# Kernel optimization log

Hardware: AMD Instinct MI355X
Metric: run time of the kernel (lower is better)

The kernel has to match this reference:

```python
import jax, jax.numpy as jnp
import numpy as np

NA, NT, E = 8000, 30000, 150000
H, C, HID = 4, 64, 64  # heads, per-head out_channels, hidden_dim
AF, TF = 32, 48


def _gat(x_src, x_dst, src, dst, W, a_src, a_dst, bias, n_dst):
    # PyG GATConv, concat=False, add_self_loops=False, eval (no dropout)
    h_src = (x_src @ W).reshape(-1, H, C)          # [Ns,H,C]
    h_dst = (x_dst @ W).reshape(-1, H, C)          # [Nd,H,C]
    al_s = jnp.sum(h_src * a_src, axis=-1)         # [Ns,H]
    al_d = jnp.sum(h_dst * a_dst, axis=-1)         # [Nd,H]
    e = jax.nn.leaky_relu(al_s[src] + al_d[dst], 0.2)  # [E,H]
    m = jax.ops.segment_max(e, dst, num_segments=n_dst)
    m = jnp.where(jnp.isfinite(m), m, 0.0)
    ex = jnp.exp(e - m[dst])
    den = jax.ops.segment_sum(ex, dst, num_segments=n_dst)
    alpha = ex / (den[dst] + 1e-16)                # per-dst softmax
    out = jax.ops.segment_sum(alpha[:, :, None] * h_src[src], dst, num_segments=n_dst)
    return jnp.mean(out, axis=1) + bias            # mean over heads + bias


def _bn(x, g, b):  # BatchNorm1d, training-mode batch stats, biased var
    mu = jnp.mean(x, axis=0)
    v = jnp.var(x, axis=0)
    return g * (x - mu) * jax.lax.rsqrt(v + 1e-5) + b


def _ln(x, g, b):
    mu = jnp.mean(x, axis=-1, keepdims=True)
    v = jnp.var(x, axis=-1, keepdims=True)
    return g * (x - mu) * jax.lax.rsqrt(v + 1e-5) + b


def setup_inputs() -> dict:
    key = jax.random.key(0)
    ks = jax.random.split(key, 40)
    n = lambda i, shp, s=0.05: jax.random.normal(ks[i], shp, jnp.float32) * s
    ri = lambda i, hi: jax.random.randint(ks[i], (E,), 0, hi, jnp.int32)
    inp = {
        'x_agent': jax.random.normal(ks[0], (NA, AF), jnp.float32),
        'x_track': jax.random.normal(ks[1], (NT, TF), jnp.float32),
        'ei_a2t1_src': ri(2, NA), 'ei_a2t1_dst': ri(3, NT),
        'ei_t2a1_src': ri(4, NT), 'ei_t2a1_dst': ri(5, NA),
        'ei_a2t2_src': ri(6, NA), 'ei_a2t2_dst': ri(7, NT),
        'ei_t2a2_src': ri(8, NT), 'ei_t2a2_dst': ri(9, NA),
        'ae_W': n(10, (AF, HID)), 'ae_b': jnp.zeros((HID,), jnp.float32),
        'te_W': n(11, (TF, HID)), 'te_b': jnp.zeros((HID,), jnp.float32),
        # stacked GATConv params: [layer=3, relation=4, ...]; rel order: a2t1,t2a1,a2t2,t2a2
        'conv_W': n(12, (3, 4, HID, H * C)),
        'conv_asrc': n(13, (3, 4, H, C)),
        'conv_adst': n(14, (3, 4, H, C)),
        'conv_bias': jnp.zeros((3, 4, C), jnp.float32),
        'bn_gamma': jnp.ones((3, 2, HID), jnp.float32),   # [layer, agent/track, HID]
        'bn_beta': jnp.zeros((3, 2, HID), jnp.float32),
        # actor heads: 0=agent_alpha,1=agent_beta,2=track_alpha,3=track_beta
        'actor_W1': n(15, (4, HID, HID // 2)), 'actor_b1': jnp.zeros((4, HID // 2), jnp.float32),
        'actor_g': jnp.ones((4, HID // 2), jnp.float32), 'actor_be': jnp.zeros((4, HID // 2), jnp.float32),
        'actor_W2': n(16, (4, HID // 2, 1)), 'actor_b2': jnp.zeros((4, 1), jnp.float32),
        # critic global value head
        'cW1': n(17, (HID * 6, HID * 2)), 'cb1': jnp.zeros((HID * 2,), jnp.float32),
        'cg1': jnp.ones((HID * 2,), jnp.float32), 'cbe1': jnp.zeros((HID * 2,), jnp.float32),
        'cW2': n(18, (HID * 2, HID)), 'cb2': jnp.zeros((HID,), jnp.float32),
        'cg2': jnp.ones((HID,), jnp.float32), 'cbe2': jnp.zeros((HID,), jnp.float32),
        'cW3': n(19, (HID, HID // 2)), 'cb3': jnp.zeros((HID // 2,), jnp.float32),
        'cW4': n(20, (HID // 2, 1)), 'cb4': jnp.zeros((1,), jnp.float32),
    }
    return inp


def _forward(x_agent, x_track,
             ei_a2t1_src, ei_a2t1_dst, ei_t2a1_src, ei_t2a1_dst,
             ei_a2t2_src, ei_a2t2_dst, ei_t2a2_src, ei_t2a2_dst,
             ae_W, ae_b, te_W, te_b,
             conv_W, conv_asrc, conv_adst, conv_bias,
             bn_gamma, bn_beta,
             actor_W1, actor_b1, actor_g, actor_be, actor_W2, actor_b2,
             cW1, cb1, cg1, cbe1, cW2, cb2, cg2, cbe2, cW3, cb3, cW4, cb4):
    xa = jax.nn.relu(x_agent @ ae_W + ae_b)
    xt = jax.nn.relu(x_track @ te_W + te_b)
    prev_a, prev_t = None, None
    for l in range(3):
        # HeteroConv aggr='mean': track <- mean(rel0, rel2); agent <- mean(rel1, rel3)
        ot = 0.5 * (_gat(xa, xt, ei_a2t1_src, ei_a2t1_dst, conv_W[l, 0], conv_asrc[l, 0], conv_adst[l, 0], conv_bias[l, 0], NT)
                    + _gat(xa, xt, ei_a2t2_src, ei_a2t2_dst, conv_W[l, 2], conv_asrc[l, 2], conv_adst[l, 2], conv_bias[l, 2], NT))
        oa = 0.5 * (_gat(xt, xa, ei_t2a1_src, ei_t2a1_dst, conv_W[l, 1], conv_asrc[l, 1], conv_adst[l, 1], conv_bias[l, 1], NA)
                    + _gat(xt, xa, ei_t2a2_src, ei_t2a2_dst, conv_W[l, 3], conv_asrc[l, 3], conv_adst[l, 3], conv_bias[l, 3], NA))
        oa = _bn(jax.nn.relu(oa), bn_gamma[l, 0], bn_beta[l, 0])
        ot = _bn(jax.nn.relu(ot), bn_gamma[l, 1], bn_beta[l, 1])
        if l > 0:  # residuals after layers 2 and 3
            oa = oa + prev_a
            ot = ot + prev_t
        prev_a, prev_t = oa, ot
        xa, xt = oa, ot

    def head(x, i):
        h = jax.nn.relu(_ln(x @ actor_W1[i] + actor_b1[i], actor_g[i], actor_be[i]))
        return jax.nn.softplus(h @ actor_W2[i] + actor_b2[i]) + 1.0

    aA, aB = head(xa, 0), head(xa, 1)
    tA, tB = head(xt, 2), head(xt, 3)
    aC = aA / (aA + aB)
    tC = tA / (tA + tB)

    # critic global value (torch.std is unbiased, ddof=1)
    g = jnp.concatenate([
        jnp.mean(xa, axis=0), jnp.max(xa, axis=0), jnp.std(xa, axis=0, ddof=1),
        jnp.mean(xt, axis=0), jnp.max(xt, axis=0), jnp.std(xt, axis=0, ddof=1)], axis=0)[None, :]
    h = jax.nn.relu(_ln(g @ cW1 + cb1, cg1, cbe1))
    h = jax.nn.relu(_ln(h @ cW2 + cb2, cg2, cbe2))
    h = jax.nn.relu(h @ cW3 + cb3)
    gv = jnp.squeeze(h @ cW4 + cb4)
    return aA, aB, aC, tA, tB, tC, gv


def reference(x_agent, x_track,
              ei_a2t1_src, ei_a2t1_dst, ei_t2a1_src, ei_t2a1_dst,
              ei_a2t2_src, ei_a2t2_dst, ei_t2a2_src, ei_t2a2_dst,
              ae_W, ae_b, te_W, te_b,
              conv_W, conv_asrc, conv_adst, conv_bias,
              bn_gamma, bn_beta,
              actor_W1, actor_b1, actor_g, actor_be, actor_W2, actor_b2,
              cW1, cb1, cg1, cbe1, cW2, cb2, cg2, cbe2, cW3, cb3, cW4, cb4):
    return _forward(x_agent, x_track,
                    ei_a2t1_src, ei_a2t1_dst, ei_t2a1_src, ei_t2a1_dst,
                    ei_a2t2_src, ei_a2t2_dst, ei_t2a2_src, ei_t2a2_dst,
                    ae_W, ae_b, te_W, te_b,
                    conv_W, conv_asrc, conv_adst, conv_bias,
                    bn_gamma, bn_beta,
                    actor_W1, actor_b1, actor_g, actor_be, actor_W2, actor_b2,
                    cW1, cb1, cg1, cbe1, cW2, cb2, cg2, cbe2, cW3, cb3, cW4, cb4)
```

## Files before the change

### kernel.cpp

```cpp
#include <hip/hip_runtime.h>
#include <math.h>

#define NAg 8000
#define NTr 30000
#define NE  150000

#define XA_OFF 0
#define XT_OFF 512000
#define H0_OFF 2432000
#define H1_OFF 4480000
#define H2_OFF 12160000
#define H3_OFF 14208000
#define BNSTB 8320000
#define WVB   8336384
#define ALS0 21888000
#define ALS1 21920000
#define ALS2 22040000
#define ALS3 22072000
#define ALD0 22192000
#define ALD1 22312000
#define ALD2 22344000
#define ALD3 22464000
#define ESRC_I 22496000
#define OAACC 23104000
#define OTACC 23616000
#define BNST 25536000
#define CST  25536256
#define ROWP_I 25536640
#define CURS_I 25656704
#define RELSTRIDE 30016

typedef unsigned short ushortT;

__device__ __forceinline__ float lrelu(float x){ return x >= 0.f ? x : 0.2f*x; }
__device__ __forceinline__ unsigned fmap(float f){ unsigned u=__float_as_uint(f); return (u&0x80000000u)? ~u : (u|0x80000000u); }
__device__ __forceinline__ float funmap(unsigned u){ return (u&0x80000000u)? __uint_as_float(u&0x7FFFFFFFu) : __uint_as_float(~u); }
__device__ __forceinline__ float softplusf(float x){ return fmaxf(x,0.f) + log1pf(expf(-fabsf(x))); }
__device__ __forceinline__ ushortT f2bf(float f){
  unsigned u = __float_as_uint(f);
  unsigned r = u + 0x7FFFu + ((u>>16)&1u);
  return (ushortT)(r>>16);
}
__device__ __forceinline__ float bf2f(ushortT s){ return __uint_as_float(((unsigned)s)<<16); }
__device__ __forceinline__ float wred64(float v){
  #pragma unroll
  for (int o=32;o;o>>=1) v += __shfl_xor(v,o);
  return v;
}
__device__ __forceinline__ float wred32(float v){
  #pragma unroll
  for (int o=16;o;o>>=1) v += __shfl_xor(v,o,32);
  return v;
}
__device__ __forceinline__ int selH(int r){ return r==0?H0_OFF: r==1?H1_OFF: r==2?H2_OFF:H3_OFF; }
__device__ __forceinline__ int selALS(int r){ return r==0?ALS0: r==1?ALS1: r==2?ALS2:ALS3; }
__device__ __forceinline__ int selALD(int r){ return r==0?ALD0: r==1?ALD1: r==2?ALD2:ALD3; }

__device__ __forceinline__ float agg_rel(const int* es, int p, int p1, const float* als,
                                         const ushortT* h16, float ad, int lane, int hh, int base) {
  float num0=0.f, num1=0.f, num2=0.f, num3=0.f, den=0.f;
  for (; p + 4 <= p1; p += 4) {
    int sa = es[p], sb = es[p+1], sc = es[p+2], sd4 = es[p+3];
    ushort4 va = *(const ushort4*)(h16 + (size_t)sa*256 + lane*4);
    ushort4 vb = *(const ushort4*)(h16 + (size_t)sb*256 + lane*4);
    ushort4 vc = *(const ushort4*)(h16 + (size_t)sc*256 + lane*4);
    ushort4 vd = *(const ushort4*)(h16 + (size_t)sd4*256 + lane*4);
    float la = als[sa*4+hh], lb = als[sb*4+hh], lc = als[sc*4+hh], ld = als[sd4*4+hh];
    float ea = __expf(lrelu(la + ad));
    float eb = __expf(lrelu(lb + ad));
    float ec = __expf(lrelu(lc + ad));
    float ed = __expf(lrelu(ld + ad));
    den += (ea+eb)+(ec+ed);
    float qa0=__shfl(ea,base), qa1=__shfl(ea,base+1), qa2=__shfl(ea,base+2), qa3=__shfl(ea,base+3);
    float qb0=__shfl(eb,base), qb1=__shfl(eb,base+1), qb2=__shfl(eb,base+2), qb3=__shfl(eb,base+3);
    float qc0=__shfl(ec,base), qc1=__shfl(ec,base+1), qc2=__shfl(ec,base+2), qc3=__shfl(ec,base+3);
    float qd0=__shfl(ed,base), qd1=__shfl(ed,base+1), qd2=__shfl(ed,base+2), qd3=__shfl(ed,base+3);
    num0 += qa0*bf2f(va.x) + qb0*bf2f(vb.x) + qc0*bf2f(vc.x) + qd0*bf2f(vd.x);
    num1 += qa1*bf2f(va.y) + qb1*bf2f(vb.y) + qc1*bf2f(vc.y) + qd1*bf2f(vd.y);
    num2 += qa2*bf2f(va.z) + qb2*bf2f(vb.z) + qc2*bf2f(vc.z) + qd2*bf2f(vd.z);
    num3 += qa3*bf2f(va.w) + qb3*bf2f(vb.w) + qc3*bf2f(vc.w) + qd3*bf2f(vd.w);
  }
  for (; p < p1; ++p) {
    int s = es[p];
    ushort4 va = *(const ushort4*)(h16 + (size_t)s*256 + lane*4);
    float e = __expf(lrelu(als[s*4 + hh] + ad));
    den += e;
    float q0 = __shfl(e, base), q1 = __shfl(e, base+1), q2 = __shfl(e, base+2), q3 = __shfl(e, base+3);
    num0 += q0*bf2f(va.x); num1 += q1*bf2f(va.y); num2 += q2*bf2f(va.z); num3 += q3*bf2f(va.w);
  }
  float rd = 1.f/(den + 1e-16f);
  float r0 = __shfl(rd, base), r1 = __shfl(rd, base+1), r2 = __shfl(rd, base+2), r3 = __shfl(rd, base+3);
  return num0*r0 + num1*r1 + num2*r2 + num3*r3;
}

__global__ __launch_bounds__(256) void k_encoder(const float* xA, const float* xT,
    const float* aeW, const float* aeB, const float* teW, const float* teB, float* ws) {
  int type = blockIdx.y;
  int N = type ? NTr : NAg;
  int t = threadIdx.x, wv = t >> 6, lane = t & 63;
  int n = blockIdx.x*4 + wv;
  int F = type ? 48 : 32;
  const float* X = type ? xT : xA;
  const float* W = type ? teW : aeW;
  const float* B = type ? teB : aeB;
  float* out = ws + (type ? XT_OFF : XA_OFF);
  __shared__ float xs[4][48];
  if (n < N && lane < F) xs[wv][lane] = X[(size_t)n*F + lane];
  __syncthreads();
  if (n >= N) return;
  float acc = B[lane];
  for (int k = 0; k < F; ++k) acc += xs[wv][k] * W[k*64 + lane];
  out[(size_t)n*64 + lane] = fmaxf(acc, 0.f);
}

__global__ __launch_bounds__(256) void k_hist(const int* d0_,const int* d1_,const int* d2_,const int* d3_,
                                              int* wsi) {
  int r = blockIdx.y;
  const int* dp = r==0? d0_ : r==1? d1_ : r==2? d2_ : d3_;
  int e = blockIdx.x*256 + threadIdx.x;
  if (e >= NE) return;
  atomicAdd(&wsi[ROWP_I + r*RELSTRIDE + dp[e]], 1);
}

__global__ __launch_bounds__(256) void k_scan(int* wsi) {
  int r = blockIdx.x;
  int n = ((r & 1) ? NAg : NTr) + 1;
  int* rp = wsi + ROWP_I + r*RELSTRIDE;
  __shared__ int part[256];
  int t = threadIdx.x;
  int chunk = (n + 255) / 256;
  int lo = t*chunk, hi = min(lo + chunk, n);
  int s = 0;
  for (int i = lo; i < hi; ++i) s += rp[i];
  part[t] = s;
  __syncthreads();
  if (t == 0) {
    int run = 0;
    for (int i = 0; i < 256; ++i) { int tm = part[i]; part[i] = run; run += tm; }
  }
  __syncthreads();
  int run = part[t];
  for (int i = lo; i < hi; ++i) { int tm = rp[i]; rp[i] = run; run += tm; }
}

__global__ __launch_bounds__(256) void k_fill(const int* s0,const int* d0_,const int* s1,const int* d1_,
    const int* s2,const int* d2_,const int* s3,const int* d3_, int* wsi) {
  int r = blockIdx.y;
  const int* sp = r==0? s0 : r==1? s1 : r==2? s2 : s3;
  const int* dp = r==0? d0_ : r==1? d1_ : r==2? d2_ : d3_;
  int e = blockIdx.x*256 + threadIdx.x;
  if (e >= NE) return;
  int d = dp[e];
  int pos = wsi[ROWP_I + r*RELSTRIDE + d] + atomicAdd(&wsi[CURS_I + r*RELSTRIDE + d], 1);
  wsi[ESRC_I + r*NE + pos] = sp[e];
}

__global__ __launch_bounds__(256) void k_wv(const float* convW, const float* convAsrc,
                                            const float* convAdst, float* ws) {
  int y = blockIdx.x, layer = blockIdx.y;
  int side = y >> 2, r = y & 3;
  const float* W  = convW + (size_t)(layer*4 + r)*64*256;
  const float* av = (side ? convAsrc : convAdst) + (size_t)(layer*4 + r)*256;
  int t = threadIdx.x;
  int k = t >> 2, h = t & 3;
  float s = 0.f;
  for (int c = 0; c < 64; ++c) s += W[k*256 + h*64 + c] * av[h*64 + c];
  ws[WVB + (size_t)(layer*8 + y)*256 + t] = s;
}

__global__ __launch_bounds__(256) void k_alx(float* ws, int layer) {
  int bid = blockIdx.x;
  int y, b0;
  if (bid < 7500)       { y = 0; b0 = bid; }
  else if (bid < 9500)  { y = 1; b0 = bid - 7500; }
  else if (bid < 17000) { y = 2; b0 = bid - 9500; }
  else if (bid < 19000) { y = 3; b0 = bid - 17000; }
  else if (bid < 21000) { y = 4; b0 = bid - 19000; }
  else if (bid < 28500) { y = 5; b0 = bid - 21000; }
  else if (bid < 30500) { y = 6; b0 = bid - 28500; }
  else                  { y = 7; b0 = bid - 30500; }
  int side = y >> 2, r = y & 3;
  int t = threadIdx.x, wv = t >> 6, lane = t & 63;
  int n = b0*4 + wv;
  const float* xv = ws + (side ? ((r & 1) ? XT_OFF : XA_OFF) : ((r & 1) ? XA_OFF : XT_OFF));
  float4 wv4 = *(const float4*)(ws + WVB + (size_t)(layer*8 + y)*256 + lane*4);
  float xk = xv[(size_t)n*64 + lane];
  float p0 = wred64(xk * wv4.x);
  float p1 = wred64(xk * wv4.y);
  float p2 = wred64(xk * wv4.z);
  float p3 = wred64(xk * wv4.w);
  if (lane == 0) {
    float4 o; o.x = p0; o.y = p1; o.z = p2; o.w = p3;
    *(float4*)(ws + (side ? selALS(r) : selALD(r)) + (size_t)n*4) = o;
  }
}

__global__ __launch_bounds__(256) void k_hgemm(const float* convW, float* ws, int layer) {
  int tile = blockIdx.x;
  int r, row0;
  if (tile < 500)        { r = 0; row0 = tile*16; }
  else if (tile < 2375)  { r = 1; row0 = (tile-500)*16; }
  else if (tile < 2875)  { r = 2; row0 = (tile-2375)*16; }
  else                   { r = 3; row0 = (tile-2875)*16; }
  const float* W  = convW + (size_t)(layer*4 + r)*64*256;
  const float* xg = ws + ((r & 1) ? XT_OFF : XA_OFF);
  ushortT* h16 = (ushortT*)(ws + selH(r));
  __shared__ float xs[16][64];
  int t = threadIdx.x;
  #pragma unroll
  for (int i = 0; i < 4; ++i) {
    int lin = i*256 + t;
    xs[lin>>6][lin&63] = xg[((size_t)row0 + (lin>>6))*64 + (lin&63)];
  }
  __syncthreads();
  int c0 = t & 63;
  int tr = t >> 6;
  float acc[4][4];
  #pragma unroll
  for (int i=0;i<4;i++){ acc[i][0]=0;acc[i][1]=0;acc[i][2]=0;acc[i][3]=0; }
  const float* Wc = W + c0;
  for (int k4 = 0; k4 < 16; ++k4) {
    float4 xv[4];
    #pragma unroll
    for (int i = 0; i < 4; ++i) xv[i] = *(const float4*)&xs[tr*4+i][k4*4];
    #pragma unroll
    for (int kk = 0; kk < 4; ++kk) {
      int k = k4*4 + kk;
      float w0 = Wc[k*256], w1 = Wc[k*256+64], w2 = Wc[k*256+128], w3 = Wc[k*256+192];
      #pragma unroll
      for (int i = 0; i < 4; ++i) {
        float x = (kk==0)?xv[i].x:(kk==1)?xv[i].y:(kk==2)?xv[i].z:xv[i].w;
        acc[i][0] += x*w0; acc[i][1] += x*w1; acc[i][2] += x*w2; acc[i][3] += x*w3;
      }
    }
  }
  #pragma unroll
  for (int i = 0; i < 4; ++i) {
    int row = row0 + tr*4 + i;
    ushort4 pk;
    pk.x = f2bf(acc[i][0]); pk.y = f2bf(acc[i][1]);
    pk.z = f2bf(acc[i][2]); pk.w = f2bf(acc[i][3]);
    *(ushort4*)(h16 + (size_t)row*256 + c0*4) = pk;
  }
}

__global__ __launch_bounds__(256) void k_agg(const float* convBias, float* ws, int layer) {
  int t = threadIdx.x, wv = t >> 6, lane = t & 63, hh = lane & 3, base = lane & ~3;
  const int* wsi = (const int*)ws;
  int bid = blockIdx.x;
  __shared__ float part[4][64];
  __shared__ float sh1[4][64];
  __shared__ float sh2[4][64];
  if (bid < 4000) {
    int node = bid*2 + (wv >> 1);
    int rr = wv & 1;
    int r = rr ? 3 : 1;
    const int* rp = wsi + ROWP_I + r*RELSTRIDE;
    const int* es = wsi + ESRC_I + r*NE;
    const float* als = ws + selALS(r);
    const ushortT* h16 = (const ushortT*)(ws + selH(r));
    float ad = (ws + selALD(r))[node*4 + hh];
    part[wv][lane] = agg_rel(es, rp[node], rp[node+1], als, h16, ad, lane, hh, base);
    __syncthreads();
    if (rr == 0) {
      float o = part[wv][lane] + part[wv+1][lane];
      float bavg = 0.5f*(convBias[(layer*4 + 1)*64 + lane] + convBias[(layer*4 + 3)*64 + lane]);
      float z = fmaxf(o*0.125f + bavg, 0.f);
      ws[OAACC + (size_t)node*64 + lane] = z;
      sh1[wv][lane] = z; sh2[wv][lane] = z*z;
    } else {
      sh1[wv][lane] = 0.f; sh2[wv][lane] = 0.f;
    }
    __syncthreads();
    if (t < 64) {
      float s1 = sh1[0][t] + sh1[1][t] + sh1[2][t] + sh1[3][t];
      float s2 = sh2[0][t] + sh2[1][t] + sh2[2][t] + sh2[3][t];
      int bucket = bid & 63;
      atomicAdd(&ws[BNSTB + bucket*256 + t], s1);
      atomicAdd(&ws[BNSTB + bucket*256 + 64 + t], s2);
    }
  } else {
    int node = (bid - 4000)*4 + wv;
    float outv = 0.f;
    #pragma unroll
    for (int rr = 0; rr < 2; ++rr) {
      int r = rr ? 2 : 0;
      const int* rp = wsi + ROWP_I + r*RELSTRIDE;
      const int* es = wsi + ESRC_I + r*NE;
      const float* als = ws + selALS(r);
      const ushortT* h16 = (const ushortT*)(ws + selH(r));
      float ad = (ws + selALD(r))[node*4 + hh];
      outv += agg_rel(es, rp[node], rp[node+1], als, h16, ad, lane, hh, base);
    }
    float bavg = 0.5f*(convBias[(layer*4 + 0)*64 + lane] + convBias[(layer*4 + 2)*64 + lane]);
    float z = fmaxf(outv*0.125f + bavg, 0.f);
    ws[OTACC + (size_t)node*64 + lane] = z;
    sh1[wv][lane] = z; sh2[wv][lane] = z*z;
    __syncthreads();
    if (t < 64) {
      float s1 = sh1[0][t] + sh1[1][t] + sh1[2][t] + sh1[3][t];
      float s2 = sh2[0][t] + sh2[1][t] + sh2[2][t] + sh2[3][t];
      int bucket = bid & 63;
      atomicAdd(&ws[BNSTB + bucket*256 + 128 + t], s1);
      atomicAdd(&ws[BNSTB + bucket*256 + 192 + t], s2);
    }
  }
}

__global__ __launch_bounds__(256) void k_bnred(float* ws) {
  int t = threadIdx.x;
  float s = 0.f;
  #pragma unroll
  for (int b = 0; b < 64; ++b) s += ws[BNSTB + b*256 + t];
  ws[BNST + t] = s;
}

__global__ __launch_bounds__(256) void k_bnnorm(const float* bnG, const float* bnB, float* ws, int layer) {
  int type = blockIdx.y;
  int N = type ? NTr : NAg;
  float* acc = ws + (type ? OTACC : OAACC);
  float* x = ws + (type ? XT_OFF : XA_OFF);
  int i = blockIdx.x*256 + threadIdx.x;
  if (i >= N*64) return;
  int c = i & 63;
  float Nf = (float)N;
  float s1 = ws[BNST + type*128 + c], s2 = ws[BNST + type*128 + 64 + c];
  float mu = s1/Nf, var = s2/Nf - mu*mu;
  float g = bnG[(layer*2 + type)*64 + c], b = bnB[(layer*2 + type)*64 + c];
  float y = g*(acc[i]-mu)*rsqrtf(var + 1e-5f) + b;
  if (layer > 0) y += x[i];
  x[i] = y;
}

__global__ __launch_bounds__(256) void k_actor(const float* aW1, const float* ab1, const float* ag,
    const float* abe, const float* aW2, const float* ab2, const float* ws, float* out) {
  int type = blockIdx.y;
  int N = type ? NTr : NAg;
  int t = threadIdx.x, wv = t >> 6, lane = t & 63;
  int p = lane >> 5, j = lane & 31;
  int n = blockIdx.x*4 + wv;
  const float* xg = ws + (type ? XT_OFF : XA_OFF);
  __shared__ float xsh[4][64];
  {
    int nn = blockIdx.x*4 + (t >> 6);
    if (nn < N) xsh[t >> 6][t & 63] = xg[(size_t)nn*64 + (t & 63)];
  }
  __syncthreads();
  if (n >= N) return;
  int i = (type ? 2 : 0) + p;
  const float* W = aW1 + i*2048 + j;
  float a0 = 0.f, a1 = 0.f, a2 = 0.f, a3 = 0.f;
  #pragma unroll
  for (int k = 0; k < 64; k += 4) {
    a0 += xsh[wv][k]   * W[k*32];
    a1 += xsh[wv][k+1] * W[(k+1)*32];
    a2 += xsh[wv][k+2] * W[(k+2)*32];
    a3 += xsh[wv][k+3] * W[(k+3)*32];
  }
  float tv = ((a0+a1)+(a2+a3)) + ab1[i*32 + j];
  float mu = wred32(tv) * (1.f/32.f);
  float dz = tv - mu;
  float var = wred32(dz*dz) * (1.f/32.f);
  float hn = fmaxf(ag[i*32+j]*dz*rsqrtf(var + 1e-5f) + abe[i*32+j], 0.f);
  float s = wred32(hn * aW2[i*32 + j]) + ab2[i];
  float val = softplusf(s) + 1.f;
  float vA = __shfl(val, 0);
  float vB = __shfl(val, 32);
  if (lane == 0) {
    int offA = type ? 24000 : 0, offB = type ? 54000 : 8000, offC = type ? 84000 : 16000;
    out[offA + n] = vA;
    out[offB + n] = vB;
    out[offC + n] = vA / (vA + vB);
  }
}

__global__ __launch_bounds__(256) void k_criticstats(float* ws) {
  int type = blockIdx.y;
  int N = type ? NTr : NAg;
  const float* x = ws + (type ? XT_OFF : XA_OFF);
  int t = threadIdx.x;
  int c = t & 63;
  float s1 = 0.f, s2 = 0.f, mx = -3.4e38f;
  for (int n = blockIdx.x*4 + (t>>6); n < N; n += gridDim.x*4) {
    float v = x[(size_t)n*64 + c];
    s1 += v; s2 += v*v; mx = fmaxf(mx, v);
  }
  __shared__ float sd[3][256];
  sd[0][t]=s1; sd[1][t]=s2; sd[2][t]=mx;
  __syncthreads();
  if (t < 64) {
    s1 = sd[0][t]+sd[0][t+64]+sd[0][t+128]+sd[0][t+192];
    s2 = sd[1][t]+sd[1][t+64]+sd[1][t+128]+sd[1][t+192];
    mx = fmaxf(fmaxf(sd[2][t],sd[2][t+64]), fmaxf(sd[2][t+128],sd[2][t+192]));
    atomicAdd(&ws[CST + type*192 + c], s1);
    atomicAdd(&ws[CST + type*192 + 64 + c], s2);
    atomicMax((unsigned*)&ws[CST + type*192 + 128 + c], fmap(mx));
  }
}

__device__ __forceinline__ float blocksum128(float v, float* red) {
  int t = threadIdx.x;
  red[t] = v; __syncthreads();
  #pragma unroll
  for (int s = 64; s > 0; s >>= 1) { if (t < s) red[t] += red[t+s]; __syncthreads(); }
  float r = red[0]; __syncthreads();
  return r;
}

__global__ __launch_bounds__(128) void k_critic(const float* cW1,const float* cb1,const float* cg1,const float* cbe1,
    const float* cW2,const float* cb2,const float* cg2,const float* cbe2,
    const float* cW3,const float* cb3,const float* cW4,const float* cb4,
    const float* ws, float* out) {
  __shared__ float g[384];
  __shared__ float h1[128];
  __shared__ float h2s[64];
  __shared__ float red[128];
  int t = threadIdx.x;
  if (t < 64) {
    #pragma unroll
    for (int type = 0; type < 2; ++type) {
      float Nf = type ? 30000.f : 8000.f;
      float s1 = ws[CST + type*192 + t];
      float s2 = ws[CST + type*192 + 64 + t];
      unsigned mu_ = __float_as_uint(ws[CST + type*192 + 128 + t]);
      float mean = s1 / Nf;
      float sd = sqrtf(fmaxf((s2 - Nf*mean*mean) / (Nf - 1.f), 0.f));
      g[type*192 + t] = mean;
      g[type*192 + 64 + t] = funmap(mu_);
      g[type*192 + 128 + t] = sd;
    }
  }
  __syncthreads();
  float v = cb1[t];
  for (int k = 0; k < 384; ++k) v += g[k] * cW1[k*128 + t];
  float mu = blocksum128(v, red) * (1.f/128.f);
  float d = v - mu;
  float var = blocksum128(d*d, red) * (1.f/128.f);
  h1[t] = fmaxf(cg1[t]*d*rsqrtf(var + 1e-5f) + cbe1[t], 0.f);
  __syncthreads();
  float v2 = 0.f;
  if (t < 64) { v2 = cb2[t]; for (int k = 0; k < 128; ++k) v2 += h1[k] * cW2[k*64 + t]; }
  float mu2 = blocksum128(t < 64 ? v2 : 0.f, red) * (1.f/64.f);
  float d2 = v2 - mu2;
  float var2 = blocksum128(t < 64 ? d2*d2 : 0.f, red) * (1.f/64.f);
  if (t < 64) h2s[t] = fmaxf(cg2[t]*d2*rsqrtf(var2 + 1e-5f) + cbe2[t], 0.f);
  __syncthreads();
  float v3 = 0.f;
  if (t < 32) {
    v3 = cb3[t];
    for (int k = 0; k < 64; ++k) v3 += h2s[k] * cW3[k*32 + t];
    v3 = fmaxf(v3, 0.f);
  }
  float s4 = blocksum128(t < 32 ? v3 * cW4[t] : 0.f, red);
  if (t == 0) out[114000] = s4 + cb4[0];
}

extern "C" void kernel_launch(void* const* d_in, const int* in_sizes, int n_in,
                              void* d_out, int out_size, void* d_ws, size_t ws_size,
                              hipStream_t stream) {
  const float* x_agent = (const float*)d_in[0];
  const float* x_track = (const float*)d_in[1];
  const int* s0 = (const int*)d_in[2]; const int* d0_ = (const int*)d_in[3];
  const int* s1 = (const int*)d_in[4]; const int* d1_ = (const int*)d_in[5];
  const int* s2 = (const int*)d_in[6]; const int* d2_ = (const int*)d_in[7];
  const int* s3 = (const int*)d_in[8]; const int* d3_ = (const int*)d_in[9];
  const float* aeW = (const float*)d_in[10]; const float* aeB = (const float*)d_in[11];
  const float* teW = (const float*)d_in[12]; const float* teB = (const float*)d_in[13];
  const float* convW    = (const float*)d_in[14];
  const float* convAsrc = (const float*)d_in[15];
  const float* convAdst = (const float*)d_in[16];
  const float* convBias = (const float*)d_in[17];
  const float* bnG = (const float*)d_in[18]; const float* bnB = (const float*)d_in[19];
  const float* aW1 = (const float*)d_in[20]; const float* ab1 = (const float*)d_in[21];
  const float* ag  = (const float*)d_in[22]; const float* abe = (const float*)d_in[23];
  const float* aW2 = (const float*)d_in[24]; const float* ab2 = (const float*)d_in[25];
  const float* cW1 = (const float*)d_in[26]; const float* cb1 = (const float*)d_in[27];
  const float* cg1 = (const float*)d_in[28]; const float* cbe1 = (const float*)d_in[29];
  const float* cW2 = (const float*)d_in[30]; const float* cb2 = (const float*)d_in[31];
  const float* cg2 = (const float*)d_in[32]; const float* cbe2 = (const float*)d_in[33];
  const float* cW3 = (const float*)d_in[34]; const float* cb3 = (const float*)d_in[35];
  const float* cW4 = (const float*)d_in[36]; const float* cb4 = (const float*)d_in[37];
  float* ws = (float*)d_ws;
  int* wsi = (int*)d_ws;
  float* out = (float*)d_out;

  hipMemsetAsync(wsi + ROWP_I, 0, (size_t)240128 * sizeof(int), stream);
  hipMemsetAsync(ws + CST, 0, (size_t)384 * sizeof(float), stream);

  k_encoder<<<dim3(7500, 2), 256, 0, stream>>>(x_agent, x_track, aeW, aeB, teW, teB, ws);

  k_hist<<<dim3(586, 4), 256, 0, stream>>>(d0_, d1_, d2_, d3_, wsi);
  k_scan<<<dim3(4), 256, 0, stream>>>(wsi);
  k_fill<<<dim3(586, 4), 256, 0, stream>>>(s0,d0_,s1,d1_,s2,d2_,s3,d3_, wsi);
  k_wv<<<dim3(8, 3), 256, 0, stream>>>(convW, convAsrc, convAdst, ws);

  for (int l = 0; l < 3; ++l) {
    hipMemsetAsync(ws + BNSTB, 0, (size_t)16384 * sizeof(float), stream);
    k_alx<<<dim3(38000), 256, 0, stream>>>(ws, l);
    k_hgemm<<<dim3(4750), 256, 0, stream>>>(convW, ws, l);
    k_agg<<<dim3(11500), 256, 0, stream>>>(convBias, ws, l);
    k_bnred<<<1, 256, 0, stream>>>(ws);
    k_bnnorm<<<dim3(7500, 2), 256, 0, stream>>>(bnG, bnB, ws, l);
  }

  k_criticstats<<<dim3(128, 2), 256, 0, stream>>>(ws);
  k_actor<<<dim3(7500, 2), 256, 0, stream>>>(aW1, ab1, ag, abe, aW2, ab2, ws, out);
  k_critic<<<1, 128, 0, stream>>>(cW1,cb1,cg1,cbe1,cW2,cb2,cg2,cbe2,cW3,cb3,cW4,cb4, ws, out);
}
```

Baseline: 668.7 us.

## Fold memsets into kernels, trim padded grids, pre-transpose conv weights

After: 659.0 us. No clear change (-1.5%).

```diff
diff --git a/kernel.cpp b/kernel.cpp
--- a/kernel.cpp
+++ b/kernel.cpp
@@ -13,6 +13,7 @@
 #define H3_OFF 14208000
 #define BNSTB 8320000
 #define WVB   8336384
+#define W2B   8342528
 #define ALS0 21888000
 #define ALS1 21920000
 #define ALS2 22040000
@@ -95,10 +96,13 @@
 
 __global__ __launch_bounds__(256) void k_encoder(const float* xA, const float* xT,
     const float* aeW, const float* aeB, const float* teW, const float* teB, float* ws) {
-  int type = blockIdx.y;
+  int bid = blockIdx.x;
+  int t = threadIdx.x, wv = t >> 6, lane = t & 63;
+  if (bid < 2 && t < 192) ws[CST + bid*192 + t] = 0.f;
+  int type, nb;
+  if (bid < 2000) { type = 0; nb = bid; } else { type = 1; nb = bid - 2000; }
   int N = type ? NTr : NAg;
-  int t = threadIdx.x, wv = t >> 6, lane = t & 63;
-  int n = blockIdx.x*4 + wv;
+  int n = nb*4 + wv;
   int F = type ? 48 : 32;
   const float* X = type ? xT : xA;
   const float* W = type ? teW : aeW;
@@ -155,21 +159,32 @@
   wsi[ESRC_I + r*NE + pos] = sp[e];
 }
 
-__global__ __launch_bounds__(256) void k_wv(const float* convW, const float* convAsrc,
-                                            const float* convAdst, float* ws) {
-  int y = blockIdx.x, layer = blockIdx.y;
-  int side = y >> 2, r = y & 3;
-  const float* W  = convW + (size_t)(layer*4 + r)*64*256;
-  const float* av = (side ? convAsrc : convAdst) + (size_t)(layer*4 + r)*256;
-  int t = threadIdx.x;
-  int k = t >> 2, h = t & 3;
-  float s = 0.f;
-  for (int c = 0; c < 64; ++c) s += W[k*256 + h*64 + c] * av[h*64 + c];
-  ws[WVB + (size_t)(layer*8 + y)*256 + t] = s;
+__global__ __launch_bounds__(256) void k_wprep2(const float* convW, const float* convAsrc,
+                                                const float* convAdst, float* ws) {
+  int lr = blockIdx.x;
+  int layer = lr >> 2, r = lr & 3;
+  const float* W = convW + (size_t)lr*64*256;
+  float* W2 = ws + W2B + (size_t)lr*64*256;
+  int t = threadIdx.x;
+  int c = t >> 2, h = t & 3;
+  for (int k = 0; k < 64; ++k) W2[k*256 + t] = W[k*256 + h*64 + c];
+  int k = t >> 2;
+  const float* ad = convAdst + (size_t)lr*256;
+  const float* as = convAsrc + (size_t)lr*256;
+  float s0 = 0.f, s1 = 0.f;
+  for (int cc = 0; cc < 64; ++cc) {
+    float w = W[k*256 + h*64 + cc];
+    s0 += w * ad[h*64 + cc];
+    s1 += w * as[h*64 + cc];
+  }
+  ws[WVB + (size_t)(layer*8 + 0*4 + r)*256 + t] = s0;
+  ws[WVB + (size_t)(layer*8 + 1*4 + r)*256 + t] = s1;
 }
 
 __global__ __launch_bounds__(256) void k_alx(float* ws, int layer) {
   int bid = blockIdx.x;
+  int t = threadIdx.x;
+  if (bid < 64) ws[BNSTB + bid*256 + t] = 0.f;
   int y, b0;
   if (bid < 7500)       { y = 0; b0 = bid; }
   else if (bid < 9500)  { y = 1; b0 = bid - 7500; }
@@ -180,7 +195,7 @@
   else if (bid < 30500) { y = 6; b0 = bid - 28500; }
   else                  { y = 7; b0 = bid - 30500; }
   int side = y >> 2, r = y & 3;
-  int t = threadIdx.x, wv = t >> 6, lane = t & 63;
+  int wv = t >> 6, lane = t & 63;
   int n = b0*4 + wv;
   const float* xv = ws + (side ? ((r & 1) ? XT_OFF : XA_OFF) : ((r & 1) ? XA_OFF : XT_OFF));
   float4 wv4 = *(const float4*)(ws + WVB + (size_t)(layer*8 + y)*256 + lane*4);
@@ -195,14 +210,14 @@
   }
 }
 
-__global__ __launch_bounds__(256) void k_hgemm(const float* convW, float* ws, int layer) {
+__global__ __launch_bounds__(256) void k_hgemm(float* ws, int layer) {
   int tile = blockIdx.x;
   int r, row0;
   if (tile < 500)        { r = 0; row0 = tile*16; }
   else if (tile < 2375)  { r = 1; row0 = (tile-500)*16; }
   else if (tile < 2875)  { r = 2; row0 = (tile-2375)*16; }
   else                   { r = 3; row0 = (tile-2875)*16; }
-  const float* W  = convW + (size_t)(layer*4 + r)*64*256;
+  const float* W2 = ws + W2B + (size_t)(layer*4 + r)*64*256;
   const float* xg = ws + ((r & 1) ? XT_OFF : XA_OFF);
   ushortT* h16 = (ushortT*)(ws + selH(r));
   __shared__ float xs[16][64];
@@ -218,7 +233,7 @@
   float acc[4][4];
   #pragma unroll
   for (int i=0;i<4;i++){ acc[i][0]=0;acc[i][1]=0;acc[i][2]=0;acc[i][3]=0; }
-  const float* Wc = W + c0;
+  const float* Wc = W2 + c0*4;
   for (int k4 = 0; k4 < 16; ++k4) {
     float4 xv[4];
     #pragma unroll
@@ -226,11 +241,11 @@
     #pragma unroll
     for (int kk = 0; kk < 4; ++kk) {
       int k = k4*4 + kk;
-      float w0 = Wc[k*256], w1 = Wc[k*256+64], w2 = Wc[k*256+128], w3 = Wc[k*256+192];
+      float4 w4 = *(const float4*)(Wc + k*256);
       #pragma unroll
       for (int i = 0; i < 4; ++i) {
         float x = (kk==0)?xv[i].x:(kk==1)?xv[i].y:(kk==2)?xv[i].z:xv[i].w;
-        acc[i][0] += x*w0; acc[i][1] += x*w1; acc[i][2] += x*w2; acc[i][3] += x*w3;
+        acc[i][0] += x*w4.x; acc[i][1] += x*w4.y; acc[i][2] += x*w4.z; acc[i][3] += x*w4.w;
       }
     }
   }
@@ -316,14 +331,14 @@
 }
 
 __global__ __launch_bounds__(256) void k_bnnorm(const float* bnG, const float* bnB, float* ws, int layer) {
-  int type = blockIdx.y;
-  int N = type ? NTr : NAg;
+  int bid = blockIdx.x;
+  int type, i;
+  if (bid < 2000) { type = 0; i = bid*256 + threadIdx.x; }
+  else            { type = 1; i = (bid - 2000)*256 + threadIdx.x; }
   float* acc = ws + (type ? OTACC : OAACC);
   float* x = ws + (type ? XT_OFF : XA_OFF);
-  int i = blockIdx.x*256 + threadIdx.x;
-  if (i >= N*64) return;
   int c = i & 63;
-  float Nf = (float)N;
+  float Nf = type ? 30000.f : 8000.f;
   float s1 = ws[BNST + type*128 + c], s2 = ws[BNST + type*128 + 64 + c];
   float mu = s1/Nf, var = s2/Nf - mu*mu;
   float g = bnG[(layer*2 + type)*64 + c], b = bnB[(layer*2 + type)*64 + c];
@@ -334,19 +349,16 @@
 
 __global__ __launch_bounds__(256) void k_actor(const float* aW1, const float* ab1, const float* ag,
     const float* abe, const float* aW2, const float* ab2, const float* ws, float* out) {
-  int type = blockIdx.y;
-  int N = type ? NTr : NAg;
+  int bid = blockIdx.x;
+  int type, nb;
+  if (bid < 2000) { type = 0; nb = bid; } else { type = 1; nb = bid - 2000; }
   int t = threadIdx.x, wv = t >> 6, lane = t & 63;
   int p = lane >> 5, j = lane & 31;
-  int n = blockIdx.x*4 + wv;
+  int n = nb*4 + wv;
   const float* xg = ws + (type ? XT_OFF : XA_OFF);
   __shared__ float xsh[4][64];
-  {
-    int nn = blockIdx.x*4 + (t >> 6);
-    if (nn < N) xsh[t >> 6][t & 63] = xg[(size_t)nn*64 + (t & 63)];
-  }
-  __syncthreads();
-  if (n >= N) return;
+  xsh[wv][lane] = xg[(size_t)n*64 + lane];
+  __syncthreads();
   int i = (type ? 2 : 0) + p;
   const float* W = aW1 + i*2048 + j;
   float a0 = 0.f, a1 = 0.f, a2 = 0.f, a3 = 0.f;
@@ -485,25 +497,23 @@
   float* out = (float*)d_out;
 
   hipMemsetAsync(wsi + ROWP_I, 0, (size_t)240128 * sizeof(int), stream);
-  hipMemsetAsync(ws + CST, 0, (size_t)384 * sizeof(float), stream);
-
-  k_encoder<<<dim3(7500, 2), 256, 0, stream>>>(x_agent, x_track, aeW, aeB, teW, teB, ws);
+
+  k_encoder<<<dim3(9500), 256, 0, stream>>>(x_agent, x_track, aeW, aeB, teW, teB, ws);
 
   k_hist<<<dim3(586, 4), 256, 0, stream>>>(d0_, d1_, d2_, d3_, wsi);
   k_scan<<<dim3(4), 256, 0, stream>>>(wsi);
   k_fill<<<dim3(586, 4), 256, 0, stream>>>(s0,d0_,s1,d1_,s2,d2_,s3,d3_, wsi);
-  k_wv<<<dim3(8, 3), 256, 0, stream>>>(convW, convAsrc, convAdst, ws);
+  k_wprep2<<<dim3(12), 256, 0, stream>>>(convW, convAsrc, convAdst, ws);
 
   for (int l = 0; l < 3; ++l) {
-    hipMemsetAsync(ws + BNSTB, 0, (size_t)16384 * sizeof(float), stream);
     k_alx<<<dim3(38000), 256, 0, stream>>>(ws, l);
-    k_hgemm<<<dim3(4750), 256, 0, stream>>>(convW, ws, l);
+    k_hgemm<<<dim3(4750), 256, 0, stream>>>(ws, l);
     k_agg<<<dim3(11500), 256, 0, stream>>>(convBias, ws, l);
     k_bnred<<<1, 256, 0, stream>>>(ws);
-    k_bnnorm<<<dim3(7500, 2), 256, 0, stream>>>(bnG, bnB, ws, l);
+    k_bnnorm<<<dim3(9500), 256, 0, stream>>>(bnG, bnB, ws, l);
   }
 
   k_criticstats<<<dim3(128, 2), 256, 0, stream>>>(ws);
-  k_actor<<<dim3(7500, 2), 256, 0, stream>>>(aW1, ab1, ag, abe, aW2, ab2, ws, out);
+  k_actor<<<dim3(9500), 256, 0, stream>>>(aW1, ab1, ag, abe, aW2, ab2, ws, out);
   k_critic<<<1, 128, 0, stream>>>(cW1,cb1,cg1,cbe1,cW2,cb2,cg2,cbe2,cW3,cb3,cW4,cb4, ws, out);
 }
```
